# Kernel optimization log

Hardware: AMD Instinct MI355X
Metric: run time of the kernel (lower is better)

Reference implementation:

```python
import jax, jax.numpy as jnp
import numpy as np

N_USERS = 100_000
N_ITEMS = 50_000
CHANNEL = 64
N_EDGES = 2_000_000
LAYERS = 3


def setup_inputs() -> dict:
    key = jax.random.key(0)
    k1, k2, k3, k4, k5 = jax.random.split(key, 5)
    user_emb = jax.random.normal(k1, (N_USERS, CHANNEL), dtype=jnp.float32) * 0.1
    item_emb = jax.random.normal(k2, (N_ITEMS, CHANNEL), dtype=jnp.float32) * 0.1
    u_idx = jax.random.randint(k3, (N_EDGES,), 0, N_USERS, dtype=jnp.int32)
    i_idx = jax.random.randint(k4, (N_EDGES,), 0, N_ITEMS, dtype=jnp.int32)
    inter_edge = jnp.stack([u_idx, i_idx], axis=0)  # [2, E]
    inter_edge_w = jax.random.uniform(k5, (N_EDGES,), dtype=jnp.float32)
    return {
        "layers_num": LAYERS,
        "user_emb": user_emb,
        "item_emb": item_emb,
        "inter_edge": inter_edge,
        "inter_edge_w": inter_edge_w,
    }


def reference(layers_num, user_emb, item_emb, inter_edge, inter_edge_w):
    """AttnHGCN.forward_ui (eval mode: no sparse dropout).

    Per layer: gather neighbor embeddings via edge index, scale by edge weight,
    scatter-sum into the other side of the bipartite graph. Residual mean over
    all layer outputs (including input embeddings).
    """
    n_users = user_emb.shape[0]
    n_items = item_emb.shape[0]
    u_idx = inter_edge[0]  # [E] user index per edge
    i_idx = inter_edge[1]  # [E] item index per edge
    w = inter_edge_w[:, None]  # [E, 1]

    u, it = user_emb, item_emb
    user_acc, item_acc = user_emb, item_emb
    for _ in range(layers_num):
        item_agg = w * it[i_idx]  # [E, C] messages item -> user
        user_agg = w * u[u_idx]   # [E, C] messages user -> item
        u = jax.ops.segment_sum(item_agg, u_idx, num_segments=n_users)
        it = jax.ops.segment_sum(user_agg, i_idx, num_segments=n_items)
        user_acc = user_acc + u
        item_acc = item_acc + it

    inv = 1.0 / (layers_num + 1)
    return item_acc * inv, user_acc * inv
```

## Files before the change

kernel.cpp:

```cpp
#include <hip/hip_runtime.h>


constexpr int N_USERS = 100000;
constexpr int N_ITEMS = 50000;
constexpr int CH      = 64;
constexpr int N_EDGES = 2000000;
constexpr int LAYERS  = 3;
constexpr int NROWS   = N_USERS + N_ITEMS;
constexpr int NDIR    = 2 * N_EDGES;

constexpr int QEDGES  = N_EDGES / 4;
constexpr int NBLK    = (QEDGES + 1023) / 1024;

constexpr int FWIN    = 512;
constexpr int FROWS   = (NROWS + FWIN - 1) / FWIN;
constexpr int NFB     = FWIN * NBLK;

constexpr long long ITEM_ELEMS = (long long)N_ITEMS * CH;
constexpr long long USER_ELEMS = (long long)N_USERS * CH;
constexpr long long TOT_ELEMS  = ITEM_ELEMS + USER_ELEMS;

typedef int      v4i __attribute__((ext_vector_type(4)));
typedef float    v4f __attribute__((ext_vector_type(4)));
typedef float    v8f __attribute__((ext_vector_type(8)));
typedef _Float16 v4h __attribute__((ext_vector_type(4)));
typedef _Float16 v8h __attribute__((ext_vector_type(8)));


__global__ __launch_bounds__(256) void scanA_kernel(
    const int* __restrict__ in, int* __restrict__ out,
    int* __restrict__ blksums, int n) {
  __shared__ int sh[256];
  int t = threadIdx.x;
  int i = blockIdx.x * 256 + t;
  int v = (i < n) ? in[i] : 0;
  int x = v;
  sh[t] = x; __syncthreads();
  for (int d = 1; d < 256; d <<= 1) {
    int add = (t >= d) ? sh[t - d] : 0;
    __syncthreads();
    x += add; sh[t] = x;
    __syncthreads();
  }
  if (i < n) out[i] = x - v;
  if (t == 255) blksums[blockIdx.x] = x;
}

__global__ __launch_bounds__(1024) void scanB_kernel(int* __restrict__ blksums, int n2) {
  __shared__ int sh[1024];
  int t = threadIdx.x;
  int v = (t < n2) ? blksums[t] : 0;
  int x = v;
  sh[t] = x; __syncthreads();
  for (int d = 1; d < 1024; d <<= 1) {
    int add = (t >= d) ? sh[t - d] : 0;
    __syncthreads();
    x += add; sh[t] = x;
    __syncthreads();
  }
  if (t < n2) blksums[t] = x - v;
}

__global__ __launch_bounds__(256) void winscanC_kernel(
    int* __restrict__ out, const int* __restrict__ blksums, int n) {
  int i = blockIdx.x * 256 + threadIdx.x;
  if (i < n) out[i] += blksums[i >> 8];
}


__global__ __launch_bounds__(1024) void bincnt1024(
    const int* __restrict__ u_idx, const int* __restrict__ i_idx,
    int* __restrict__ blkfine) {
  __shared__ int cnt[FWIN];
  const int t = threadIdx.x;
  if (t < FWIN) cnt[t] = 0;
  __syncthreads();
  int q = blockIdx.x * 1024 + t;
  if (q < QEDGES) {
    v4i u  = *(const v4i*)(u_idx + 4 * (long long)q);
    v4i it = *(const v4i*)(i_idx + 4 * (long long)q);
    atomicAdd(&cnt[u.x / FROWS], 1);
    atomicAdd(&cnt[u.y / FROWS], 1);
    atomicAdd(&cnt[u.z / FROWS], 1);
    atomicAdd(&cnt[u.w / FROWS], 1);
    atomicAdd(&cnt[(N_USERS + it.x) / FROWS], 1);
    atomicAdd(&cnt[(N_USERS + it.y) / FROWS], 1);
    atomicAdd(&cnt[(N_USERS + it.z) / FROWS], 1);
    atomicAdd(&cnt[(N_USERS + it.w) / FROWS], 1);
  }
  __syncthreads();
  if (t < FWIN) blkfine[(long long)t * NBLK + blockIdx.x] = cnt[t];
}

__global__ __launch_bounds__(256) void fineoff_ext(
    const int* __restrict__ blkfine, int* __restrict__ fineoff) {
  int i = blockIdx.x * 256 + threadIdx.x;
  if (i < FWIN) fineoff[i] = blkfine[(long long)i * NBLK];
  if (i == FWIN) fineoff[FWIN] = NDIR;
}

__global__ __launch_bounds__(1024) void segwrite1024(
    const int* __restrict__ u_idx, const int* __restrict__ i_idx,
    const float* __restrict__ wv, const int* __restrict__ blkfine,
    int* __restrict__ segkey, _Float16* __restrict__ segw) {
  extern __shared__ char smem[];
  int*            skey = (int*)smem;
  _Float16*       sw   = (_Float16*)(skey + 8192);
  unsigned short* sfin = (unsigned short*)(sw + 8192);
  int*            cnt  = (int*)(sfin + 8192);

  const int t   = threadIdx.x;
  const int blk = blockIdx.x;
  if (t < FWIN) cnt[t] = 0;
  __syncthreads();

  int q = blk * 1024 + t;
  bool valid = (q < QEDGES);
  int key8[8], fin8[8], rank8[8];
  _Float16 hw8[8];
  if (valid) {
    v4i u  = *(const v4i*)(u_idx + 4 * (long long)q);
    v4i it = *(const v4i*)(i_idx + 4 * (long long)q);
    v4f w  = *(const v4f*)(wv + 4 * (long long)q);
    int rows[8], srcs[8];
    float ws[8];
    rows[0] = u.x; rows[1] = u.y; rows[2] = u.z; rows[3] = u.w;
    srcs[0] = it.x; srcs[1] = it.y; srcs[2] = it.z; srcs[3] = it.w;
    rows[4] = N_USERS + it.x; rows[5] = N_USERS + it.y;
    rows[6] = N_USERS + it.z; rows[7] = N_USERS + it.w;
    srcs[4] = u.x; srcs[5] = u.y; srcs[6] = u.z; srcs[7] = u.w;
    ws[0] = w.x; ws[1] = w.y; ws[2] = w.z; ws[3] = w.w;
    ws[4] = w.x; ws[5] = w.y; ws[6] = w.z; ws[7] = w.w;
#pragma unroll
    for (int k = 0; k < 8; ++k) {
      int fin = rows[k] / FROWS;
      int dl  = rows[k] - fin * FROWS;
      fin8[k]  = fin;
      key8[k]  = (dl << 18) | ((k >= 4) ? (1 << 17) : 0) | srcs[k];
      hw8[k]   = (_Float16)ws[k];
      rank8[k] = atomicAdd(&cnt[fin], 1);
    }
  }
  __syncthreads();

  int v = 0, x = 0;
  if (t < FWIN) { v = cnt[t]; x = v; }
  for (int d = 1; d < FWIN; d <<= 1) {
    int add = (t < FWIN && t >= d) ? cnt[t - d] : 0;
    __syncthreads();
    if (t < FWIN) { x += add; cnt[t] = x; }
    __syncthreads();
  }
  if (t < FWIN) cnt[t] = x - v;
  __syncthreads();

  if (valid) {
#pragma unroll
    for (int k = 0; k < 8; ++k) {
      int slot = cnt[fin8[k]] + rank8[k];
      skey[slot] = key8[k];
      sw[slot]   = hw8[k];
      sfin[slot] = (unsigned short)fin8[k];
    }
  }
  __syncthreads();

  const int ecount = 8 * min(1024, QEDGES - blk * 1024);
  for (int j = t; j < ecount; j += 1024) {
    int f = sfin[j];
    int gpos = blkfine[(long long)f * NBLK + blk] + (j - cnt[f]);
    segkey[gpos] = skey[j];
    segw[gpos]   = sw[j];
  }
}

__global__ __launch_bounds__(1024) void win_sort512(
    const int* __restrict__ segkey, const _Float16* __restrict__ segw,
    const int* __restrict__ fineoff, int* __restrict__ row_ptr,
    int* __restrict__ csrk, _Float16* __restrict__ csrw) {
  __shared__ int hist[FWIN];
  const int w   = blockIdx.x;
  const int wlo = w * FROWS;
  const int wsz = min(FROWS, NROWS - wlo);
  const int s0  = fineoff[w], s1 = fineoff[w + 1];
  const int t   = threadIdx.x;

  if (t < FWIN) hist[t] = 0;
  __syncthreads();

  for (int idx = s0 + t; idx < s1; idx += 1024)
    atomicAdd(&hist[((unsigned)segkey[idx]) >> 18], 1);
  __syncthreads();

  int v = 0, x = 0;
  if (t < FWIN) { v = hist[t]; x = v; }
  for (int d = 1; d < FWIN; d <<= 1) {
    int add = (t < FWIN && t >= d) ? hist[t - d] : 0;
    __syncthreads();
    if (t < FWIN) { x += add; hist[t] = x; }
    __syncthreads();
  }
  __syncthreads();
  int base = x - v;
  if (t < wsz) row_ptr[wlo + t] = s0 + base;
  if (w == FWIN - 1 && t == 0) row_ptr[NROWS] = NDIR;
  if (t < FWIN) hist[t] = s0 + base;
  __syncthreads();

  for (int idx = s0 + t; idx < s1; idx += 1024) {
    int key = segkey[idx];
    int p = atomicAdd(&hist[((unsigned)key) >> 18], 1);
    csrk[p] = key & 0x1FFFF;
    csrw[p] = segw[idx];
  }
}

__global__ __launch_bounds__(256) void cvt_tab(
    const float* __restrict__ it, const float* __restrict__ u,
    _Float16* __restrict__ t0) {
  long long i = (long long)blockIdx.x * 256 + threadIdx.x;
  if (i >= TOT_ELEMS / 4) return;
  long long e = i * 4;
  const float* src = (e < ITEM_ELEMS) ? (it + e) : (u + (e - ITEM_ELEMS));
  v4f f = *(const v4f*)src;
  v4h h = {(_Float16)f.x, (_Float16)f.y, (_Float16)f.z, (_Float16)f.w};
  *(v4h*)(t0 + e) = h;
}

template <int MODE>
__global__ __launch_bounds__(256) void gather_fused(
    const _Float16* __restrict__ tab,
    _Float16* __restrict__ dst,
    float* __restrict__ out,
    const int* __restrict__ csrk, const _Float16* __restrict__ csrw,
    const int* __restrict__ row_ptr) {
  int row = blockIdx.x * 4 + (threadIdx.x >> 6);
  if (row >= NROWS) return;
  int lane = threadIdx.x & 63;
  int slot = lane >> 3;
  int c8   = (lane & 7) * 8;

  const _Float16* gtab;
  const _Float16* erow = nullptr;
  _Float16* drow = nullptr;
  float* orow;
  if (row < N_USERS) {
    gtab = tab;
    orow = out + ITEM_ELEMS + (long long)row * CH;
    if (MODE < 2)  drow = dst + ITEM_ELEMS + (long long)row * CH;
    if (MODE == 0) erow = tab + ITEM_ELEMS + (long long)row * CH;
  } else {
    int r = row - N_USERS;
    gtab = tab + ITEM_ELEMS;
    orow = out + (long long)r * CH;
    if (MODE < 2)  drow = dst + (long long)r * CH;
    if (MODE == 0) erow = tab + (long long)r * CH;
  }

  int beg = row_ptr[row], end = row_ptr[row + 1];
  float acc[8];
#pragma unroll
  for (int k = 0; k < 8; ++k) acc[k] = 0.f;
  int j = beg + slot;
  for (; j + 8 < end; j += 16) {
    int k0 = csrk[j];
    int k1 = csrk[j + 8];
    float w0 = (float)csrw[j];
    float w1 = (float)csrw[j + 8];
    v8h h0 = *(const v8h*)(gtab + (long long)k0 * CH + c8);
    v8h h1 = *(const v8h*)(gtab + (long long)k1 * CH + c8);
#pragma unroll
    for (int k = 0; k < 8; ++k) acc[k] += w0 * (float)h0[k];
#pragma unroll
    for (int k = 0; k < 8; ++k) acc[k] += w1 * (float)h1[k];
  }
  if (j < end) {
    int k0 = csrk[j];
    float we = (float)csrw[j];
    v8h h = *(const v8h*)(gtab + (long long)k0 * CH + c8);
#pragma unroll
    for (int k = 0; k < 8; ++k) acc[k] += we * (float)h[k];
  }
#pragma unroll
  for (int off = 8; off < 64; off <<= 1) {
#pragma unroll
    for (int k = 0; k < 8; ++k) acc[k] += __shfl_xor(acc[k], off, 64);
  }
  if (slot == 0) {
    if (MODE < 2) {
      v8h hd;
#pragma unroll
      for (int k = 0; k < 8; ++k) hd[k] = (_Float16)acc[k];
      *(v8h*)(drow + c8) = hd;
    }
    if (MODE == 0) {
      v8h e8 = *(const v8h*)(erow + c8);
      v8f o;
#pragma unroll
      for (int k = 0; k < 8; ++k) o[k] = (float)e8[k] + acc[k];
      *(v8f*)(orow + c8) = o;
    } else if (MODE == 1) {
      v8f o = *(const v8f*)(orow + c8);
#pragma unroll
      for (int k = 0; k < 8; ++k) o[k] += acc[k];
      *(v8f*)(orow + c8) = o;
    } else {
      const float s = 1.0f / (LAYERS + 1);
      v8f o = *(const v8f*)(orow + c8);
#pragma unroll
      for (int k = 0; k < 8; ++k) o[k] = (o[k] + acc[k]) * s;
      *(v8f*)(orow + c8) = o;
    }
  }
}


__global__ __launch_bounds__(256) void atomic_scatter_kernel(
    const float* __restrict__ src, float* __restrict__ dst,
    const int* __restrict__ u_idx, const int* __restrict__ i_idx,
    const float* __restrict__ w) {
  long long tid = (long long)blockIdx.x * blockDim.x + threadIdx.x;
  int edge = (int)(tid >> 4);
  if (edge >= N_EDGES) return;
  int c = ((int)tid & 15) * 4;
  int ui = u_idx[edge], ii = i_idx[edge];
  float we = w[edge];
  float4 itv = *(const float4*)(src + (long long)ii * CH + c);
  float4 uv  = *(const float4*)(src + ITEM_ELEMS + (long long)ui * CH + c);
  float* ud = dst + ITEM_ELEMS + (long long)ui * CH + c;
  float* id = dst + (long long)ii * CH + c;
  unsafeAtomicAdd(ud + 0, we * itv.x);
  unsafeAtomicAdd(ud + 1, we * itv.y);
  unsafeAtomicAdd(ud + 2, we * itv.z);
  unsafeAtomicAdd(ud + 3, we * itv.w);
  unsafeAtomicAdd(id + 0, we * uv.x);
  unsafeAtomicAdd(id + 1, we * uv.y);
  unsafeAtomicAdd(id + 2, we * uv.z);
  unsafeAtomicAdd(id + 3, we * uv.w);
}

__global__ __launch_bounds__(256) void add_scale_kernel(
    float* __restrict__ acc, const float* __restrict__ add, float s, long long n4) {
  long long i = (long long)blockIdx.x * blockDim.x + threadIdx.x;
  if (i >= n4) return;
  float4 a = ((const float4*)acc)[i];
  float4 b = ((const float4*)add)[i];
  a.x = (a.x + b.x) * s;
  a.y = (a.y + b.y) * s;
  a.z = (a.z + b.z) * s;
  a.w = (a.w + b.w) * s;
  ((float4*)acc)[i] = a;
}

extern "C" void kernel_launch(void* const* d_in, const int* in_sizes, int n_in,
                              void* d_out, int out_size, void* d_ws, size_t ws_size,
                              hipStream_t stream) {
  const float* user_emb = (const float*)d_in[1];
  const float* item_emb = (const float*)d_in[2];
  const int*   edges    = (const int*)d_in[3];
  const int*   u_idx    = edges;
  const int*   i_idx    = edges + N_EDGES;
  const float* w        = (const float*)d_in[4];

  float* out = (float*)d_out;

  float* buf_a   = (float*)d_ws;
  float* buf_b   = buf_a + TOT_ELEMS;
  float* csr_rg  = buf_b + TOT_ELEMS;
  int*   ibase   = (int*)(csr_rg + 2 * (size_t)NDIR / 1);
  const size_t needed =
      ((size_t)2 * TOT_ELEMS + 2 * (size_t)NDIR + 3 * (size_t)NROWS + 1 + 1024) * 4;

  int*      segkey  = (int*)buf_a;
  _Float16* segw    = (_Float16*)(segkey + NDIR);
  int*      csrk    = (int*)csr_rg;
  _Float16* csrw    = (_Float16*)(csrk + NDIR);
  int*      fineoff = ibase;
  int*      row_ptr = ibase + NROWS;
  int*      blkfine = (int*)buf_b;
  int*      bsumsF  = blkfine + NFB;
  _Float16* t0 = (_Float16*)buf_a;
  _Float16* t1 = t0 + TOT_ELEMS;
  _Float16* t2 = (_Float16*)buf_b;

  if (ws_size >= needed) {
    bincnt1024<<<NBLK, 1024, 0, stream>>>(u_idx, i_idx, blkfine);
    const int nbF = (NFB + 255) / 256;
    scanA_kernel<<<nbF, 256, 0, stream>>>(blkfine, blkfine, bsumsF, NFB);
    scanB_kernel<<<1, 1024, 0, stream>>>(bsumsF, nbF);
    winscanC_kernel<<<nbF, 256, 0, stream>>>(blkfine, bsumsF, NFB);
    fineoff_ext<<<3, 256, 0, stream>>>(blkfine, fineoff);
    const size_t seg_smem = 8192 * 4 + 8192 * 2 + 8192 * 2 + FWIN * 4;
    segwrite1024<<<NBLK, 1024, seg_smem, stream>>>(
        u_idx, i_idx, w, blkfine, segkey, segw);

    win_sort512<<<FWIN, 1024, 0, stream>>>(
        segkey, segw, fineoff, row_ptr, csrk, csrw);

    const int cvt_blocks = (int)((TOT_ELEMS / 4 + 255) / 256);
    cvt_tab<<<cvt_blocks, 256, 0, stream>>>(item_emb, user_emb, t0);

    const int gather_blocks = (NROWS + 3) / 4;
    gather_fused<0><<<gather_blocks, 256, 0, stream>>>(
        t0, t1, out, csrk, csrw, row_ptr);
    gather_fused<1><<<gather_blocks, 256, 0, stream>>>(
        t1, t2, out, csrk, csrw, row_ptr);
    gather_fused<2><<<gather_blocks, 256, 0, stream>>>(
        t2, nullptr, out, csrk, csrw, row_ptr);
  } else {
    const size_t item_bytes = (size_t)ITEM_ELEMS * sizeof(float);
    const size_t user_bytes = (size_t)USER_ELEMS * sizeof(float);
    hipMemcpyAsync(buf_a,              item_emb, item_bytes, hipMemcpyDeviceToDevice, stream);
    hipMemcpyAsync(buf_a + ITEM_ELEMS, user_emb, user_bytes, hipMemcpyDeviceToDevice, stream);
    hipMemcpyAsync(out,                item_emb, item_bytes, hipMemcpyDeviceToDevice, stream);
    hipMemcpyAsync(out + ITEM_ELEMS,   user_emb, user_bytes, hipMemcpyDeviceToDevice, stream);
    const long long st = (long long)N_EDGES * 16;
    const int sb = (int)((st + 255) / 256);
    const long long n4 = TOT_ELEMS / 4;
    const int add_blocks = (int)((n4 + 255) / 256);
    float* src = buf_a;
    float* dst = buf_b;
    for (int l = 0; l < LAYERS; ++l) {
      hipMemsetAsync(dst, 0, (size_t)TOT_ELEMS * sizeof(float), stream);
      atomic_scatter_kernel<<<sb, 256, 0, stream>>>(src, dst, u_idx, i_idx, w);
      const float s = (l == LAYERS - 1) ? (1.0f / (LAYERS + 1)) : 1.0f;
      add_scale_kernel<<<add_blocks, 256, 0, stream>>>(out, dst, s, n4);
      float* t = src; src = dst; dst = t;
    }
  }
}
```

Before: 412.1 us.

## Pack CSR index and weight into one word, defer residual sum

Packs each CSR entry's 17-bit neighbour index and the low 15 bits of its fp16 weight into one 32-bit word, dropping the separate weight array. The window sort now stages keys and weights in LDS when a window fits, instead of reading global memory twice. The fp32 output is no longer read and rewritten in every layer. The last layer instead sums the fp16 layer tables t0, t1, t2 plus its own accumulator and writes the output once. This cuts CSR and output memory traffic, but the residual now uses fp16 copies of the input embeddings and relies on edge weights being non-negative.

```diff
diff --git a/kernel.cpp b/kernel.cpp
--- a/kernel.cpp
+++ b/kernel.cpp
@@ -16,6 +16,8 @@
 constexpr int FROWS   = (NROWS + FWIN - 1) / FWIN;
 constexpr int NFB     = FWIN * NBLK;
 
+constexpr int WCAP    = 9216;
+
 constexpr long long ITEM_ELEMS = (long long)N_ITEMS * CH;
 constexpr long long USER_ELEMS = (long long)N_USERS * CH;
 constexpr long long TOT_ELEMS  = ITEM_ELEMS + USER_ELEMS;
@@ -25,6 +27,18 @@
 typedef float    v8f __attribute__((ext_vector_type(8)));
 typedef _Float16 v4h __attribute__((ext_vector_type(4)));
 typedef _Float16 v8h __attribute__((ext_vector_type(8)));
+
+static __device__ __forceinline__ float w15_to_f(unsigned pk) {
+  unsigned short us = (unsigned short)(pk & 0x7FFF);
+  _Float16 h;
+  __builtin_memcpy(&h, &us, 2);
+  return (float)h;
+}
+static __device__ __forceinline__ unsigned pack_sw(int src, _Float16 hw) {
+  unsigned short us;
+  __builtin_memcpy(&us, &hw, 2);
+  return ((unsigned)src << 15) | (us & 0x7FFF);
+}
 
 
 __global__ __launch_bounds__(256) void scanA_kernel(
@@ -177,19 +191,36 @@
 __global__ __launch_bounds__(1024) void win_sort512(
     const int* __restrict__ segkey, const _Float16* __restrict__ segw,
     const int* __restrict__ fineoff, int* __restrict__ row_ptr,
-    int* __restrict__ csrk, _Float16* __restrict__ csrw) {
-  __shared__ int hist[FWIN];
+    unsigned* __restrict__ csrp) {
+  __shared__ unsigned        lkey[WCAP];
+  __shared__ unsigned short  lwb[WCAP];
+  __shared__ int             hist[FWIN];
   const int w   = blockIdx.x;
   const int wlo = w * FROWS;
   const int wsz = min(FROWS, NROWS - wlo);
   const int s0  = fineoff[w], s1 = fineoff[w + 1];
+  const int n   = s1 - s0;
+  const bool inlds = (n <= WCAP);
   const int t   = threadIdx.x;
 
   if (t < FWIN) hist[t] = 0;
-  __syncthreads();
-
-  for (int idx = s0 + t; idx < s1; idx += 1024)
-    atomicAdd(&hist[((unsigned)segkey[idx]) >> 18], 1);
+  if (inlds) {
+    for (int i = t; i < n; i += 1024) {
+      lkey[i] = (unsigned)segkey[s0 + i];
+      _Float16 h = segw[s0 + i];
+      unsigned short us;
+      __builtin_memcpy(&us, &h, 2);
+      lwb[i] = us;
+    }
+  }
+  __syncthreads();
+
+  if (inlds) {
+    for (int i = t; i < n; i += 1024) atomicAdd(&hist[lkey[i] >> 18], 1);
+  } else {
+    for (int i = t; i < n; i += 1024)
+      atomicAdd(&hist[((unsigned)segkey[s0 + i]) >> 18], 1);
+  }
   __syncthreads();
 
   int v = 0, x = 0;
@@ -207,11 +238,18 @@
   if (t < FWIN) hist[t] = s0 + base;
   __syncthreads();
 
-  for (int idx = s0 + t; idx < s1; idx += 1024) {
-    int key = segkey[idx];
-    int p = atomicAdd(&hist[((unsigned)key) >> 18], 1);
-    csrk[p] = key & 0x1FFFF;
-    csrw[p] = segw[idx];
+  if (inlds) {
+    for (int i = t; i < n; i += 1024) {
+      unsigned key = lkey[i];
+      int p = atomicAdd(&hist[key >> 18], 1);
+      csrp[p] = ((key & 0x1FFFFu) << 15) | (lwb[i] & 0x7FFF);
+    }
+  } else {
+    for (int i = t; i < n; i += 1024) {
+      unsigned key = (unsigned)segkey[s0 + i];
+      int p = atomicAdd(&hist[key >> 18], 1);
+      csrp[p] = pack_sw(key & 0x1FFFF, segw[s0 + i]);
+    }
   }
 }
 
@@ -231,8 +269,10 @@
 __global__ __launch_bounds__(256) void gather_fused(
     const _Float16* __restrict__ tab,
     _Float16* __restrict__ dst,
+    const _Float16* __restrict__ e0,
+    const _Float16* __restrict__ e1,
     float* __restrict__ out,
-    const int* __restrict__ csrk, const _Float16* __restrict__ csrw,
+    const unsigned* __restrict__ csrp,
     const int* __restrict__ row_ptr) {
   int row = blockIdx.x * 4 + (threadIdx.x >> 6);
   if (row >= NROWS) return;
@@ -241,20 +281,13 @@
   int c8   = (lane & 7) * 8;
 
   const _Float16* gtab;
-  const _Float16* erow = nullptr;
-  _Float16* drow = nullptr;
-  float* orow;
+  long long own;
   if (row < N_USERS) {
     gtab = tab;
-    orow = out + ITEM_ELEMS + (long long)row * CH;
-    if (MODE < 2)  drow = dst + ITEM_ELEMS + (long long)row * CH;
-    if (MODE == 0) erow = tab + ITEM_ELEMS + (long long)row * CH;
+    own  = ITEM_ELEMS + (long long)row * CH;
   } else {
-    int r = row - N_USERS;
     gtab = tab + ITEM_ELEMS;
-    orow = out + (long long)r * CH;
-    if (MODE < 2)  drow = dst + (long long)r * CH;
-    if (MODE == 0) erow = tab + (long long)r * CH;
+    own  = (long long)(row - N_USERS) * CH;
   }
 
   int beg = row_ptr[row], end = row_ptr[row + 1];
@@ -263,21 +296,21 @@
   for (int k = 0; k < 8; ++k) acc[k] = 0.f;
   int j = beg + slot;
   for (; j + 8 < end; j += 16) {
-    int k0 = csrk[j];
-    int k1 = csrk[j + 8];
-    float w0 = (float)csrw[j];
-    float w1 = (float)csrw[j + 8];
-    v8h h0 = *(const v8h*)(gtab + (long long)k0 * CH + c8);
-    v8h h1 = *(const v8h*)(gtab + (long long)k1 * CH + c8);
+    unsigned p0 = csrp[j];
+    unsigned p1 = csrp[j + 8];
+    v8h h0 = *(const v8h*)(gtab + (long long)(p0 >> 15) * CH + c8);
+    v8h h1 = *(const v8h*)(gtab + (long long)(p1 >> 15) * CH + c8);
+    float w0 = w15_to_f(p0);
+    float w1 = w15_to_f(p1);
 #pragma unroll
     for (int k = 0; k < 8; ++k) acc[k] += w0 * (float)h0[k];
 #pragma unroll
     for (int k = 0; k < 8; ++k) acc[k] += w1 * (float)h1[k];
   }
   if (j < end) {
-    int k0 = csrk[j];
-    float we = (float)csrw[j];
-    v8h h = *(const v8h*)(gtab + (long long)k0 * CH + c8);
+    unsigned p0 = csrp[j];
+    float we = w15_to_f(p0);
+    v8h h = *(const v8h*)(gtab + (long long)(p0 >> 15) * CH + c8);
 #pragma unroll
     for (int k = 0; k < 8; ++k) acc[k] += we * (float)h[k];
   }
@@ -291,25 +324,17 @@
       v8h hd;
 #pragma unroll
       for (int k = 0; k < 8; ++k) hd[k] = (_Float16)acc[k];
-      *(v8h*)(drow + c8) = hd;
-    }
-    if (MODE == 0) {
-      v8h e8 = *(const v8h*)(erow + c8);
-      v8f o;
-#pragma unroll
-      for (int k = 0; k < 8; ++k) o[k] = (float)e8[k] + acc[k];
-      *(v8f*)(orow + c8) = o;
-    } else if (MODE == 1) {
-      v8f o = *(const v8f*)(orow + c8);
-#pragma unroll
-      for (int k = 0; k < 8; ++k) o[k] += acc[k];
-      *(v8f*)(orow + c8) = o;
+      *(v8h*)(dst + own + c8) = hd;
     } else {
       const float s = 1.0f / (LAYERS + 1);
-      v8f o = *(const v8f*)(orow + c8);
-#pragma unroll
-      for (int k = 0; k < 8; ++k) o[k] = (o[k] + acc[k]) * s;
-      *(v8f*)(orow + c8) = o;
+      v8h a0 = *(const v8h*)(e0 + own + c8);
+      v8h a1 = *(const v8h*)(e1 + own + c8);
+      v8h a2 = *(const v8h*)(tab + own + c8);
+      v8f o;
+#pragma unroll
+      for (int k = 0; k < 8; ++k)
+        o[k] = ((float)a0[k] + (float)a1[k] + (float)a2[k] + acc[k]) * s;
+      *(v8f*)(out + own + c8) = o;
     }
   }
 }
@@ -367,14 +392,13 @@
   float* buf_a   = (float*)d_ws;
   float* buf_b   = buf_a + TOT_ELEMS;
   float* csr_rg  = buf_b + TOT_ELEMS;
-  int*   ibase   = (int*)(csr_rg + 2 * (size_t)NDIR / 1);
+  int*   ibase   = (int*)(csr_rg + 2 * (size_t)NDIR);
   const size_t needed =
       ((size_t)2 * TOT_ELEMS + 2 * (size_t)NDIR + 3 * (size_t)NROWS + 1 + 1024) * 4;
 
   int*      segkey  = (int*)buf_a;
   _Float16* segw    = (_Float16*)(segkey + NDIR);
-  int*      csrk    = (int*)csr_rg;
-  _Float16* csrw    = (_Float16*)(csrk + NDIR);
+  unsigned* csrp    = (unsigned*)csr_rg;
   int*      fineoff = ibase;
   int*      row_ptr = ibase + NROWS;
   int*      blkfine = (int*)buf_b;
@@ -395,18 +419,18 @@
         u_idx, i_idx, w, blkfine, segkey, segw);
 
     win_sort512<<<FWIN, 1024, 0, stream>>>(
-        segkey, segw, fineoff, row_ptr, csrk, csrw);
+        segkey, segw, fineoff, row_ptr, csrp);
 
     const int cvt_blocks = (int)((TOT_ELEMS / 4 + 255) / 256);
     cvt_tab<<<cvt_blocks, 256, 0, stream>>>(item_emb, user_emb, t0);
 
     const int gather_blocks = (NROWS + 3) / 4;
     gather_fused<0><<<gather_blocks, 256, 0, stream>>>(
-        t0, t1, out, csrk, csrw, row_ptr);
+        t0, t1, nullptr, nullptr, nullptr, csrp, row_ptr);
     gather_fused<1><<<gather_blocks, 256, 0, stream>>>(
-        t1, t2, out, csrk, csrw, row_ptr);
+        t1, t2, nullptr, nullptr, nullptr, csrp, row_ptr);
     gather_fused<2><<<gather_blocks, 256, 0, stream>>>(
-        t2, nullptr, out, csrk, csrw, row_ptr);
+        t2, nullptr, t0, t1, out, csrp, row_ptr);
   } else {
     const size_t item_bytes = (size_t)ITEM_ELEMS * sizeof(float);
     const size_t user_bytes = (size_t)USER_ELEMS * sizeof(float);
```

New measurement: 378.0 us. 1.09x faster.
